# Kernel tuning notes

Measured on AMD Instinct MI355X. Metric: run time of the kernel, lower is better.

Reference implementation:

```python
import jax, jax.numpy as jnp
import numpy as np
from jax import lax

HEADS = 4
NEG_SLOPE = 0.2


def _layernorm(x, g, b, eps=1e-5):
    m = x.mean(-1, keepdims=True)
    v = ((x - m) ** 2).mean(-1, keepdims=True)
    return (x - m) * lax.rsqrt(v + eps) * g + b


def setup_inputs() -> dict:
    key = jax.random.key(0)
    ks = jax.random.split(key, 10)
    B, N, T, H, E, ED, K = 1, 1000, 32, 128, 16000, 16, 3
    s_h = 1.0 / np.sqrt(H)
    s_e = 1.0 / np.sqrt(ED)
    return {
        "x": jax.random.normal(ks[0], (B, N, T, H), jnp.float32),
        "edge_index": jax.random.randint(ks[1], (2, E), 0, N, dtype=jnp.int32),
        "edge_attr": jax.random.normal(ks[2], (E, ED), jnp.float32),
        "conv_w": jax.random.normal(ks[3], (H, H, K), jnp.float32) * (1.0 / np.sqrt(H * K)),
        "conv_b": jnp.zeros((H,), jnp.float32),
        "ln1_g": jnp.ones((H,), jnp.float32),
        "ln1_b": jnp.zeros((H,), jnp.float32),
        "Wl": jax.random.normal(ks[4], (H, H), jnp.float32) * s_h,
        "Wr": jax.random.normal(ks[5], (H, H), jnp.float32) * s_h,
        "We": jax.random.normal(ks[6], (ED, H), jnp.float32) * s_e,
        "att": jax.random.normal(ks[7], (HEADS, H // HEADS), jnp.float32) * s_h,
        "gat_b": jnp.zeros((H,), jnp.float32),
        "ln2_g": jnp.ones((H,), jnp.float32),
        "ln2_b": jnp.zeros((H,), jnp.float32),
    }


def reference(x, edge_index, edge_attr, conv_w, conv_b, ln1_g, ln1_b,
              Wl, Wr, We, att, gat_b, ln2_g, ln2_b):
    B, N, T, H = x.shape
    K = HEADS
    D = H // K
    E = edge_attr.shape[0]

    # ---- temporal sub-block: per-node Conv1d over time ('same' padding) ----
    xt = x.reshape(B * N, T, H).transpose(0, 2, 1)            # [BN, H, T]
    y = lax.conv_general_dilated(xt, conv_w, (1,), 'SAME',
                                 dimension_numbers=('NCH', 'OIH', 'NCH'))
    y = y + conv_b[None, :, None]
    y = y.transpose(0, 2, 1).reshape(B, N, T, H)
    x = _layernorm(x + y, ln1_g, ln1_b)

    # ---- spatial sub-block: GATv2 at every timestep (mega-batch of G graphs) ----
    G = B * T
    xs = x.transpose(0, 2, 1, 3).reshape(G, N, H)             # [G, N, H]

    # add self-loops, fill_value='mean' (mean of incoming edge attrs per node)
    dst0 = edge_index[1]
    cnt = jax.ops.segment_sum(jnp.ones((E,), edge_attr.dtype), dst0, num_segments=N)
    loop_attr = jax.ops.segment_sum(edge_attr, dst0, num_segments=N) / jnp.maximum(cnt, 1.0)[:, None]
    ea = jnp.concatenate([edge_attr, loop_attr], axis=0)       # [E+N, ED]
    loops = jnp.arange(N, dtype=edge_index.dtype)
    src = jnp.concatenate([edge_index[0], loops])
    dst = jnp.concatenate([edge_index[1], loops])

    gl = jnp.einsum('gnh,hkd->gnkd', xs, Wl.reshape(H, K, D))  # source transform
    gr = jnp.einsum('gnh,hkd->gnkd', xs, Wr.reshape(H, K, D))  # target transform
    ee = jnp.einsum('ef,fkd->ekd', ea, We.reshape(-1, K, D))   # edge transform

    e_src = jnp.swapaxes(gl[:, src], 0, 1)                     # [E', G, K, D]
    e_dst = jnp.swapaxes(gr[:, dst], 0, 1)                     # [E', G, K, D]
    s = jax.nn.leaky_relu(e_src + e_dst + ee[:, None], NEG_SLOPE)
    logits = jnp.einsum('egkd,kd->egk', s, att)                # [E', G, K]

    # scatter-softmax over incoming edges per target node (self-loops => non-empty)
    mx = jax.ops.segment_max(logits, dst, num_segments=N)[dst]
    ex = jnp.exp(logits - mx)
    den = jax.ops.segment_sum(ex, dst, num_segments=N)[dst]
    alpha = ex / den

    aggr = jax.ops.segment_sum(e_src * alpha[..., None], dst, num_segments=N)  # [N, G, K, D]
    out = jnp.swapaxes(aggr, 0, 1).reshape(G, N, H) + gat_b

    out = out.reshape(B, T, N, H).transpose(0, 2, 1, 3)        # back to (B, N, T, H)
    return _layernorm(x + out, ln2_g, ln2_b)
```

## Files before the change

### kernel.cpp

```cpp
#include <hip/hip_runtime.h>
#include <math.h>

#define N_NODES 1000
#define T_STEPS 32
#define H_DIM   128
#define E_EDGES 16000
#define ED_DIM  16
#define G_GRAPHS 32
#define EP_EDGES (E_EDGES + N_NODES)
#define NEG_SLOPE 0.2f
#define LN_EPS 1e-5f

typedef __attribute__((ext_vector_type(8))) short bf16x8;
typedef __attribute__((ext_vector_type(16))) float f32x16;
typedef __attribute__((ext_vector_type(4))) float f32x4;
typedef __attribute__((ext_vector_type(4))) unsigned u32x4;
typedef unsigned short u16;

__device__ inline short f2bf(float f) {
    unsigned u = __float_as_uint(f);
    u = (u + 0x7FFFu + ((u >> 16) & 1u)) >> 16;
    return (short)u;
}
__device__ inline float bflo(unsigned u) { return __uint_as_float(u << 16); }
__device__ inline float bfhi(unsigned u) { return __uint_as_float(u & 0xFFFF0000u); }

__global__ __launch_bounds__(1024) void k_prep(
    const float* __restrict__ conv_w, const float* __restrict__ Wl,
    const float* __restrict__ Wr, const int* __restrict__ dst,
    short* __restrict__ wc, short* __restrict__ wg,
    int* __restrict__ cnt, int* __restrict__ offs, int* __restrict__ csr) {
    int b = blockIdx.x;
    if (b < 80) {
        int i = b * 1024 + threadIdx.x;
        if (i < 4 * 24 * 64 * 8) {
            int r = i & 7, lane = (i >> 3) & 63;
            int t = i >> 9;
            int kstep = t % 24, ct = t / 24;
            int k = kstep >> 3, hs = kstep & 7;
            int hi = hs * 16 + ((lane >> 5) << 3) + r;
            int o = ct * 32 + (lane & 31);
            wc[i] = f2bf(conv_w[(o * H_DIM + hi) * 3 + k]);
        } else {
            int j = i - 4 * 24 * 64 * 8;
            int r = j & 7, lane = (j >> 3) & 63;
            int ks = (j >> 9) & 7, ct = j >> 12;
            int hi = ks * 16 + ((lane >> 5) << 3) + r;
            int o = ct * 32 + (lane & 31);
            wg[j] = f2bf(o < H_DIM ? Wl[hi * H_DIM + o] : Wr[hi * H_DIM + o - H_DIM]);
        }
        return;
    }
    __shared__ int sm[1024];
    __shared__ int sl[1024];
    int t = threadIdx.x;
    sm[t] = 0;
    __syncthreads();
    for (int e = t; e < E_EDGES; e += 1024) atomicAdd(&sm[dst[e]], 1);
    __syncthreads();
    int v = (t < N_NODES) ? sm[t] : 0;
    if (t < N_NODES) cnt[t] = v;
    for (int s = 1; s < 1024; s <<= 1) {
        __syncthreads();
        int a = (t >= s) ? sm[t - s] : 0;
        __syncthreads();
        sm[t] += a;
    }
    __syncthreads();
    if (t < N_NODES) offs[t + 1] = sm[t];
    if (t == 0) offs[0] = 0;
    sl[t] = sm[t] - v;
    __syncthreads();
    for (int e = t; e < E_EDGES; e += 1024) {
        int d = dst[e];
        int s = atomicAdd(&sl[d], 1);
        csr[s] = e;
    }
}

__global__ __launch_bounds__(256) void k_graphprep(
    const float* __restrict__ edge_attr, const float* __restrict__ We,
    int* __restrict__ csr, const int* __restrict__ offs, const int* __restrict__ cnt,
    u16* __restrict__ ee) {
    int b = blockIdx.x;
    int tid = threadIdx.x;
    if (b < N_NODES) {
        __shared__ int buf[128];
        __shared__ float laf[16];
        int n = b;
        int off = offs[n], deg = cnt[n];
        bool fast = (deg <= 64);
        if (fast) {
            if (tid < 64) {
                int v = (tid < deg) ? csr[off + tid] : 0x7FFFFFFF;
                int rank = 0;
#pragma unroll
                for (int j = 0; j < 64; ++j) {
                    int vj = __shfl(v, j);
                    rank += (vj < v) ? 1 : 0;
                }
                if (tid < deg) buf[rank] = v;
            }
        } else {
            for (int i = tid; i < deg && i < 128; i += 256) buf[i] = csr[off + i];
        }
        __syncthreads();
        if (!fast && tid == 0) {
            int dd = deg < 128 ? deg : 128;
            for (int i = 1; i < dd; ++i) {
                int key = buf[i], j = i - 1;
                while (j >= 0 && buf[j] > key) { buf[j + 1] = buf[j]; --j; }
                buf[j + 1] = key;
            }
        }
        __syncthreads();
        if (tid < deg && tid < 128) csr[off + tid] = buf[tid];
        if (tid < 64) {
            int q = tid >> 4, f = tid & 15;
            float a = 0.f;
            for (int i = q; i < deg; i += 4) a += edge_attr[buf[i] * ED_DIM + f];
            a += __shfl_xor(a, 16);
            a += __shfl_xor(a, 32);
            if (tid < 16) laf[tid] = a / fmaxf((float)deg, 1.0f);
        }
        __syncthreads();
        if (tid < H_DIM) {
            float acc = 0.f;
#pragma unroll
            for (int f = 0; f < ED_DIM; ++f) acc += laf[f] * We[f * H_DIM + tid];
            ee[(size_t)(E_EDGES + n) * H_DIM + tid] = (u16)f2bf(acc);
        }
    } else {
        int e = (b - N_NODES) * 2 + (tid >> 7);
        int h = tid & 127;
        if (e >= E_EDGES) return;
        const float* ea = &edge_attr[e * ED_DIM];
        float acc = 0.f;
#pragma unroll
        for (int f = 0; f < ED_DIM; ++f) acc += ea[f] * We[f * H_DIM + h];
        ee[(size_t)e * H_DIM + h] = (u16)f2bf(acc);
    }
}

__global__ __launch_bounds__(256) void k_temporal(
    const float* __restrict__ x, const short* __restrict__ wc, const short* __restrict__ wg,
    const float* __restrict__ conv_b, const float* __restrict__ ln1_g,
    const float* __restrict__ ln1_b, float* __restrict__ x1,
    u16* __restrict__ gl, u16* __restrict__ gr) {
    __shared__ __align__(16) short xb[34 * 136];
    __shared__ float yb[32 * 132];
    int n = blockIdx.x;
    int tid = threadIdx.x;
    int w = tid >> 6, lane = tid & 63;
    int arow = lane & 31;
    int aks = (lane >> 5) << 3;

    {
        const float4* xs4 = (const float4*)(x + (size_t)n * T_STEPS * H_DIM);
        for (int i4 = tid; i4 < T_STEPS * H_DIM / 4; i4 += 256) {
            float4 v = xs4[i4];
            int t = i4 >> 5, h = (i4 * 4) & 127;
            uint2 pp;
            pp.x = (unsigned)(unsigned short)f2bf(v.x) | ((unsigned)(unsigned short)f2bf(v.y) << 16);
            pp.y = (unsigned)(unsigned short)f2bf(v.z) | ((unsigned)(unsigned short)f2bf(v.w) << 16);
            *(uint2*)&xb[(t + 1) * 136 + h] = pp;
        }
        if (tid < 68) {
            ((unsigned*)xb)[tid] = 0u;
            ((unsigned*)(xb + 33 * 136))[tid] = 0u;
        }
    }
    __syncthreads();

    f32x16 acc = {};
    for (int kk = 0; kk < 3; ++kk) {
#pragma unroll
        for (int hs = 0; hs < 8; ++hs) {
            int kstep = kk * 8 + hs;
            bf16x8 a = *(const bf16x8*)&xb[(arow + kk) * 136 + hs * 16 + aks];
            bf16x8 b = *(const bf16x8*)&wc[((w * 24 + kstep) * 64 + lane) * 8];
            acc = __builtin_amdgcn_mfma_f32_32x32x16_bf16(a, b, acc, 0, 0, 0);
        }
    }
    {
        int oc = w * 32 + (lane & 31);
        float cb = conv_b[oc];
#pragma unroll
        for (int r = 0; r < 16; ++r) {
            int t = (r & 3) + 8 * (r >> 2) + 4 * (lane >> 5);
            yb[t * 132 + oc] = acc[r] + cb;
        }
    }
    __syncthreads();

    for (int t = w; t < T_STEPS; t += 4) {
        float r0 = x[((size_t)n * T_STEPS + t) * H_DIM + lane] + yb[t * 132 + lane];
        float r1 = x[((size_t)n * T_STEPS + t) * H_DIM + lane + 64] + yb[t * 132 + lane + 64];
        float s = r0 + r1, s2 = r0 * r0 + r1 * r1;
#pragma unroll
        for (int mm = 1; mm < 64; mm <<= 1) {
            s += __shfl_xor(s, mm);
            s2 += __shfl_xor(s2, mm);
        }
        float mean = s * (1.f / 128.f);
        float var = s2 * (1.f / 128.f) - mean * mean;
        float rs = rsqrtf(var + LN_EPS);
        float o0 = (r0 - mean) * rs * ln1_g[lane] + ln1_b[lane];
        float o1 = (r1 - mean) * rs * ln1_g[lane + 64] + ln1_b[lane + 64];
        x1[((size_t)n * T_STEPS + t) * H_DIM + lane] = o0;
        x1[((size_t)n * T_STEPS + t) * H_DIM + lane + 64] = o1;
        xb[t * 136 + lane] = f2bf(o0);
        xb[t * 136 + lane + 64] = f2bf(o1);
    }
    __syncthreads();

    f32x16 cl = {}, cr = {};
#pragma unroll
    for (int ks = 0; ks < 8; ++ks) {
        bf16x8 a = *(const bf16x8*)&xb[arow * 136 + ks * 16 + aks];
        bf16x8 b0 = *(const bf16x8*)&wg[(((2 * w) * 8 + ks) * 64 + lane) * 8];
        bf16x8 b1 = *(const bf16x8*)&wg[(((2 * w + 1) * 8 + ks) * 64 + lane) * 8];
        cl = __builtin_amdgcn_mfma_f32_32x32x16_bf16(a, b0, cl, 0, 0, 0);
        cr = __builtin_amdgcn_mfma_f32_32x32x16_bf16(a, b1, cr, 0, 0, 0);
    }
    {
        int o0 = 64 * w + (lane & 31);
        u16* d = (w < 2) ? gl : gr;
        int oo0 = (w < 2) ? o0 : o0 - 128;
        int oo1 = oo0 + 32;
#pragma unroll
        for (int r = 0; r < 16; ++r) {
            int t = (r & 3) + 8 * (r >> 2) + 4 * (lane >> 5);
            d[((size_t)t * N_NODES + n) * H_DIM + oo0] = (u16)f2bf(cl[r]);
            d[((size_t)t * N_NODES + n) * H_DIM + oo1] = (u16)f2bf(cr[r]);
        }
    }
}

__global__ __launch_bounds__(128) void k_gat(
    const u16* __restrict__ gl, const u16* __restrict__ gr, const u16* __restrict__ ee,
    const int* __restrict__ src_arr, const int* __restrict__ csr,
    const int* __restrict__ offs, const int* __restrict__ cnt,
    const float* __restrict__ att, const float* __restrict__ gat_b,
    const float* __restrict__ x1, const float* __restrict__ ln2_g,
    const float* __restrict__ ln2_b, float* __restrict__ out) {
    int bid = blockIdx.x;
    int q = bid & 3;
    int n = bid >> 2;
    int tid = threadIdx.x;
    int gs = tid >> 4;
    int r = tid & 15;
    int h0 = ((r >> 2) << 5) + ((r & 3) << 3);
    int g = q + 4 * gs;

    __shared__ int es[64], ss[64];
    int off = offs[n], deg = cnt[n];
    int tot = deg + 1;

    float av[8], grv[8];
    {
        float4 a0 = *(const float4*)&att[h0];
        float4 a1 = *(const float4*)&att[h0 + 4];
        av[0] = a0.x; av[1] = a0.y; av[2] = a0.z; av[3] = a0.w;
        av[4] = a1.x; av[5] = a1.y; av[6] = a1.z; av[7] = a1.w;
        u32x4 g4 = *(const u32x4*)&gr[((size_t)g * N_NODES + n) * H_DIM + h0];
        grv[0] = bflo(g4.x); grv[1] = bfhi(g4.x); grv[2] = bflo(g4.y); grv[3] = bfhi(g4.y);
        grv[4] = bflo(g4.z); grv[5] = bfhi(g4.z); grv[6] = bflo(g4.w); grv[7] = bfhi(g4.w);
    }
    const u16* glg = gl + (size_t)g * N_NODES * H_DIM + h0;
    const u16* eeh = ee + h0;

    float m = -INFINITY, l = 0.f;
    float ac[8] = {0.f, 0.f, 0.f, 0.f, 0.f, 0.f, 0.f, 0.f};

    for (int base = 0; base < tot; base += 64) {
        int c = min(64, tot - base);
        __syncthreads();
        if (tid < c) {
            int i = base + tid;
            int e = (i < deg) ? csr[off + i] : (E_EDGES + n);
            es[tid] = e;
            ss[tid] = (i < deg) ? src_arr[e] : n;
        }
        __syncthreads();
        u32x4 gv4 = *(const u32x4*)&glg[(size_t)ss[0] * H_DIM];
        u32x4 ev4 = __builtin_nontemporal_load((const u32x4*)&eeh[(size_t)es[0] * H_DIM]);
        for (int i = 0; i < c; ++i) {
            u32x4 gc = gv4, ec = ev4;
            if (i + 1 < c) {
                gv4 = *(const u32x4*)&glg[(size_t)ss[i + 1] * H_DIM];
                ev4 = __builtin_nontemporal_load((const u32x4*)&eeh[(size_t)es[i + 1] * H_DIM]);
            }
            float gv[8];
            gv[0] = bflo(gc.x); gv[1] = bfhi(gc.x); gv[2] = bflo(gc.y); gv[3] = bfhi(gc.y);
            gv[4] = bflo(gc.z); gv[5] = bfhi(gc.z); gv[6] = bflo(gc.w); gv[7] = bfhi(gc.w);
            float p = 0.f;
#pragma unroll
            for (int j = 0; j < 8; ++j) {
                float evj = (j & 1) ? bfhi(((const unsigned*)&ec)[j >> 1])
                                    : bflo(((const unsigned*)&ec)[j >> 1]);
                float sf = gv[j] + grv[j] + evj;
                sf = fmaxf(sf, NEG_SLOPE * sf);
                p = fmaf(sf, av[j], p);
            }
            p += __shfl_xor(p, 1);
            p += __shfl_xor(p, 2);
            float mn = fmaxf(m, p);
            float sc = __expf(m - mn);
            float wq = __expf(p - mn);
            l = l * sc + wq;
#pragma unroll
            for (int j = 0; j < 8; ++j) ac[j] = ac[j] * sc + wq * gv[j];
            m = mn;
        }
    }

    float linv = 1.0f / l;
    size_t ob = ((size_t)n * T_STEPS + g) * H_DIM + h0;
    float4 x0 = *(const float4*)&x1[ob];
    float4 x1v = *(const float4*)&x1[ob + 4];
    float4 gb0 = *(const float4*)&gat_b[h0];
    float4 gb1 = *(const float4*)&gat_b[h0 + 4];
    float rv[8];
    rv[0] = x0.x + ac[0] * linv + gb0.x;
    rv[1] = x0.y + ac[1] * linv + gb0.y;
    rv[2] = x0.z + ac[2] * linv + gb0.z;
    rv[3] = x0.w + ac[3] * linv + gb0.w;
    rv[4] = x1v.x + ac[4] * linv + gb1.x;
    rv[5] = x1v.y + ac[5] * linv + gb1.y;
    rv[6] = x1v.z + ac[6] * linv + gb1.z;
    rv[7] = x1v.w + ac[7] * linv + gb1.w;
    float s1 = 0.f, s2v = 0.f;
#pragma unroll
    for (int j = 0; j < 8; ++j) { s1 += rv[j]; s2v += rv[j] * rv[j]; }
#pragma unroll
    for (int mm = 1; mm < 16; mm <<= 1) {
        s1 += __shfl_xor(s1, mm);
        s2v += __shfl_xor(s2v, mm);
    }
    float mean = s1 * (1.f / 128.f);
    float var = s2v * (1.f / 128.f) - mean * mean;
    float rs = rsqrtf(var + LN_EPS);
    float4 g20 = *(const float4*)&ln2_g[h0];
    float4 g21 = *(const float4*)&ln2_g[h0 + 4];
    float4 b20 = *(const float4*)&ln2_b[h0];
    float4 b21 = *(const float4*)&ln2_b[h0 + 4];
    f32x4 o0, o1;
    o0.x = (rv[0] - mean) * rs * g20.x + b20.x;
    o0.y = (rv[1] - mean) * rs * g20.y + b20.y;
    o0.z = (rv[2] - mean) * rs * g20.z + b20.z;
    o0.w = (rv[3] - mean) * rs * g20.w + b20.w;
    o1.x = (rv[4] - mean) * rs * g21.x + b21.x;
    o1.y = (rv[5] - mean) * rs * g21.y + b21.y;
    o1.z = (rv[6] - mean) * rs * g21.z + b21.z;
    o1.w = (rv[7] - mean) * rs * g21.w + b21.w;
    __builtin_nontemporal_store(o0, (f32x4*)&out[ob]);
    __builtin_nontemporal_store(o1, (f32x4*)&out[ob + 4]);
}

extern "C" void kernel_launch(void* const* d_in, const int* in_sizes, int n_in,
                              void* d_out, int out_size, void* d_ws, size_t ws_size,
                              hipStream_t stream) {
    const float* x         = (const float*)d_in[0];
    const int*   ei        = (const int*)d_in[1];
    const float* edge_attr = (const float*)d_in[2];
    const float* conv_w    = (const float*)d_in[3];
    const float* conv_b    = (const float*)d_in[4];
    const float* ln1_g     = (const float*)d_in[5];
    const float* ln1_b     = (const float*)d_in[6];
    const float* Wl        = (const float*)d_in[7];
    const float* Wr        = (const float*)d_in[8];
    const float* We        = (const float*)d_in[9];
    const float* att       = (const float*)d_in[10];
    const float* gat_b     = (const float*)d_in[11];
    const float* ln2_g     = (const float*)d_in[12];
    const float* ln2_b     = (const float*)d_in[13];
    float* out = (float*)d_out;

    const int* src = ei;
    const int* dst = ei + E_EDGES;

    float* x1   = (float*)d_ws;
    u16*   glb  = (u16*)(x1 + 4096000);
    u16*   grb  = glb + 4096000;
    u16*   eeb  = grb + 4096000;
    float* la   = (float*)(eeb + 2176000);
    int* ibase  = (int*)(la + 16000);
    int* cnt    = ibase;
    int* cnt2   = ibase + 1000;
    int* offs   = ibase + 2000;
    int* csr    = ibase + 3001;
    short* wc   = (short*)(ibase + 19008);
    short* wg   = wc + 49152;

    k_prep<<<81, 1024, 0, stream>>>(conv_w, Wl, Wr, dst, wc, wg, cnt, offs, csr);
    k_graphprep<<<N_NODES + (E_EDGES + 1) / 2, 256, 0, stream>>>(edge_attr, We, csr, offs,
                                                                 cnt, eeb);
    k_temporal<<<N_NODES, 256, 0, stream>>>(x, wc, wg, conv_b, ln1_g, ln1_b, x1, glb, grb);
    k_gat<<<4 * N_NODES, 128, 0, stream>>>(glb, grb, eeb, src, csr, offs, cnt,
                                           att, gat_b, x1, ln2_g, ln2_b, out);
}
```

Measured before the change: 84.57 us.

## Store LN1 output in bf16 and stage gl/gr through LDS for vector stores

The layernorm-1 output x1 is now kept as bf16 (copied from the shared bf16 tile) instead of fp32, halving its write in the temporal kernel and its read in the GAT kernel. The gl/gr projection results are first staged in shared memory, then written to global memory as 16-byte rows instead of scattered 2-byte stores. The workspace layout is compacted to match. This trades extra syncthreads and LDS traffic, plus some precision loss on the residual term, for fewer and wider global memory transactions.

```diff
diff --git a/kernel.cpp b/kernel.cpp
--- a/kernel.cpp
+++ b/kernel.cpp
@@ -145,10 +145,10 @@
 __global__ __launch_bounds__(256) void k_temporal(
     const float* __restrict__ x, const short* __restrict__ wc, const short* __restrict__ wg,
     const float* __restrict__ conv_b, const float* __restrict__ ln1_g,
-    const float* __restrict__ ln1_b, float* __restrict__ x1,
+    const float* __restrict__ ln1_b, u16* __restrict__ x1b,
     u16* __restrict__ gl, u16* __restrict__ gr) {
     __shared__ __align__(16) short xb[34 * 136];
-    __shared__ float yb[32 * 132];
+    __shared__ __align__(16) float yb[32 * 136];
     int n = blockIdx.x;
     int tid = threadIdx.x;
     int w = tid >> 6, lane = tid & 63;
@@ -188,14 +188,14 @@
 #pragma unroll
         for (int r = 0; r < 16; ++r) {
             int t = (r & 3) + 8 * (r >> 2) + 4 * (lane >> 5);
-            yb[t * 132 + oc] = acc[r] + cb;
+            yb[t * 136 + oc] = acc[r] + cb;
         }
     }
     __syncthreads();
 
     for (int t = w; t < T_STEPS; t += 4) {
-        float r0 = x[((size_t)n * T_STEPS + t) * H_DIM + lane] + yb[t * 132 + lane];
-        float r1 = x[((size_t)n * T_STEPS + t) * H_DIM + lane + 64] + yb[t * 132 + lane + 64];
+        float r0 = x[((size_t)n * T_STEPS + t) * H_DIM + lane] + yb[t * 136 + lane];
+        float r1 = x[((size_t)n * T_STEPS + t) * H_DIM + lane + 64] + yb[t * 136 + lane + 64];
         float s = r0 + r1, s2 = r0 * r0 + r1 * r1;
 #pragma unroll
         for (int mm = 1; mm < 64; mm <<= 1) {
@@ -207,12 +207,16 @@
         float rs = rsqrtf(var + LN_EPS);
         float o0 = (r0 - mean) * rs * ln1_g[lane] + ln1_b[lane];
         float o1 = (r1 - mean) * rs * ln1_g[lane + 64] + ln1_b[lane + 64];
-        x1[((size_t)n * T_STEPS + t) * H_DIM + lane] = o0;
-        x1[((size_t)n * T_STEPS + t) * H_DIM + lane + 64] = o1;
         xb[t * 136 + lane] = f2bf(o0);
         xb[t * 136 + lane + 64] = f2bf(o1);
     }
     __syncthreads();
+
+    for (int c = tid; c < 512; c += 256) {
+        int t = c >> 4, p = c & 15;
+        u32x4 v = *(const u32x4*)&xb[t * 136 + p * 8];
+        *(u32x4*)&x1b[((size_t)n * T_STEPS + t) * H_DIM + p * 8] = v;
+    }
 
     f32x16 cl = {}, cr = {};
 #pragma unroll
@@ -223,16 +227,26 @@
         cl = __builtin_amdgcn_mfma_f32_32x32x16_bf16(a, b0, cl, 0, 0, 0);
         cr = __builtin_amdgcn_mfma_f32_32x32x16_bf16(a, b1, cr, 0, 0, 0);
     }
+    __syncthreads();
     {
-        int o0 = 64 * w + (lane & 31);
-        u16* d = (w < 2) ? gl : gr;
-        int oo0 = (w < 2) ? o0 : o0 - 128;
-        int oo1 = oo0 + 32;
+        u16* st = (u16*)yb;
+        int m = w >> 1;
+        int c0 = (w & 1) * 64 + (lane & 31);
 #pragma unroll
         for (int r = 0; r < 16; ++r) {
             int t = (r & 3) + 8 * (r >> 2) + 4 * (lane >> 5);
-            d[((size_t)t * N_NODES + n) * H_DIM + oo0] = (u16)f2bf(cl[r]);
-            d[((size_t)t * N_NODES + n) * H_DIM + oo1] = (u16)f2bf(cr[r]);
+            st[(m * 32 + t) * 136 + c0] = (u16)f2bf(cl[r]);
+            st[(m * 32 + t) * 136 + c0 + 32] = (u16)f2bf(cr[r]);
+        }
+    }
+    __syncthreads();
+    {
+        const u16* st = (const u16*)yb;
+        for (int c = tid; c < 1024; c += 256) {
+            int m = c >> 9, t = (c >> 4) & 31, p = c & 15;
+            u32x4 v = *(const u32x4*)&st[(m * 32 + t) * 136 + p * 8];
+            u16* d = m ? gr : gl;
+            *(u32x4*)&d[((size_t)t * N_NODES + n) * H_DIM + p * 8] = v;
         }
     }
 }
@@ -242,7 +256,7 @@
     const int* __restrict__ src_arr, const int* __restrict__ csr,
     const int* __restrict__ offs, const int* __restrict__ cnt,
     const float* __restrict__ att, const float* __restrict__ gat_b,
-    const float* __restrict__ x1, const float* __restrict__ ln2_g,
+    const u16* __restrict__ x1b, const float* __restrict__ ln2_g,
     const float* __restrict__ ln2_b, float* __restrict__ out) {
     int bid = blockIdx.x;
     int q = bid & 3;
@@ -317,22 +331,21 @@
 
     float linv = 1.0f / l;
     size_t ob = ((size_t)n * T_STEPS + g) * H_DIM + h0;
-    float4 x0 = *(const float4*)&x1[ob];
-    float4 x1v = *(const float4*)&x1[ob + 4];
     float4 gb0 = *(const float4*)&gat_b[h0];
     float4 gb1 = *(const float4*)&gat_b[h0 + 4];
+    u32x4 xv = *(const u32x4*)&x1b[ob];
+    float xr[8];
+    xr[0] = bflo(xv.x); xr[1] = bfhi(xv.x); xr[2] = bflo(xv.y); xr[3] = bfhi(xv.y);
+    xr[4] = bflo(xv.z); xr[5] = bfhi(xv.z); xr[6] = bflo(xv.w); xr[7] = bfhi(xv.w);
+    float gbv[8] = {gb0.x, gb0.y, gb0.z, gb0.w, gb1.x, gb1.y, gb1.z, gb1.w};
     float rv[8];
-    rv[0] = x0.x + ac[0] * linv + gb0.x;
-    rv[1] = x0.y + ac[1] * linv + gb0.y;
-    rv[2] = x0.z + ac[2] * linv + gb0.z;
-    rv[3] = x0.w + ac[3] * linv + gb0.w;
-    rv[4] = x1v.x + ac[4] * linv + gb1.x;
-    rv[5] = x1v.y + ac[5] * linv + gb1.y;
-    rv[6] = x1v.z + ac[6] * linv + gb1.z;
-    rv[7] = x1v.w + ac[7] * linv + gb1.w;
     float s1 = 0.f, s2v = 0.f;
 #pragma unroll
-    for (int j = 0; j < 8; ++j) { s1 += rv[j]; s2v += rv[j] * rv[j]; }
+    for (int j = 0; j < 8; ++j) {
+        rv[j] = xr[j] + ac[j] * linv + gbv[j];
+        s1 += rv[j];
+        s2v += rv[j] * rv[j];
+    }
 #pragma unroll
     for (int mm = 1; mm < 16; mm <<= 1) {
         s1 += __shfl_xor(s1, mm);
@@ -380,23 +393,21 @@
     const int* src = ei;
     const int* dst = ei + E_EDGES;
 
-    float* x1   = (float*)d_ws;
-    u16*   glb  = (u16*)(x1 + 4096000);
-    u16*   grb  = glb + 4096000;
-    u16*   eeb  = grb + 4096000;
-    float* la   = (float*)(eeb + 2176000);
-    int* ibase  = (int*)(la + 16000);
+    u16* x1b    = (u16*)d_ws;
+    u16* glb    = x1b + 4096000;
+    u16* grb    = glb + 4096000;
+    u16* eeb    = grb + 4096000;
+    int* ibase  = (int*)(eeb + 2176000);
     int* cnt    = ibase;
-    int* cnt2   = ibase + 1000;
-    int* offs   = ibase + 2000;
-    int* csr    = ibase + 3001;
-    short* wc   = (short*)(ibase + 19008);
+    int* offs   = ibase + 1000;
+    int* csr    = ibase + 2001;
+    short* wc   = (short*)(ibase + 18008);
     short* wg   = wc + 49152;
 
     k_prep<<<81, 1024, 0, stream>>>(conv_w, Wl, Wr, dst, wc, wg, cnt, offs, csr);
     k_graphprep<<<N_NODES + (E_EDGES + 1) / 2, 256, 0, stream>>>(edge_attr, We, csr, offs,
                                                                  cnt, eeb);
-    k_temporal<<<N_NODES, 256, 0, stream>>>(x, wc, wg, conv_b, ln1_g, ln1_b, x1, glb, grb);
+    k_temporal<<<N_NODES, 256, 0, stream>>>(x, wc, wg, conv_b, ln1_g, ln1_b, x1b, glb, grb);
     k_gat<<<4 * N_NODES, 128, 0, stream>>>(glb, grb, eeb, src, csr, offs, cnt,
-                                           att, gat_b, x1, ln2_g, ln2_b, out);
-}
+                                           att, gat_b, x1b, ln2_g, ln2_b, out);
+}
```

Result: no change. 84.47 us (-0.1%).
